# Optimization experiments

Hardware: AMD Instinct MI355X
Metric: run time of the kernel (lower is better)

The kernel has to match this reference:

```python
import jax, jax.numpy as jnp
from jax import lax
import numpy as np

N_QUBITS = 8
N_LAYERS = 7
DIM = 2 ** N_QUBITS  # 256 amplitudes


def _conv(x, w, b, stride, pad):
    y = lax.conv_general_dilated(x, w, (stride, stride), [(pad, pad), (pad, pad)],
                                 dimension_numbers=("NCHW", "OIHW", "NCHW"))
    return y + b[None, :, None, None]


def _adaptive_pool2(x):
    # AdaptiveAvgPool2d(2) on 7x7 input: bins [0:4) and [3:7) per spatial dim (overlap at idx 3)
    bins = [(0, 4), (3, 7)]
    rows = [x[:, :, s:e, :].mean(axis=2) for s, e in bins]  # each (B,C,7)
    return jnp.stack([jnp.stack([r[:, :, s:e].mean(axis=2) for s, e in bins], axis=-1)
                      for r in rows], axis=-2)  # (B,C,2,2)


def _qsim(feat, weights):
    # Batched 8-qubit statevector simulation. PennyLane default.qubit ordering:
    # wire 0 is the most-significant axis. RY and CNOT are real matrices and the
    # amplitude-embedded state is real, so the state stays real throughout.
    norm = jnp.linalg.norm(feat, axis=1, keepdims=True)
    state = feat / jnp.maximum(norm, 1e-12)  # AmplitudeEmbedding(normalize=True), (B,256)
    B = state.shape[0]
    for layer in range(N_LAYERS):
        for q in range(N_QUBITS):  # RY(weights[layer,q]) on wire q
            theta = weights[layer, q]
            c, s = jnp.cos(theta / 2), jnp.sin(theta / 2)
            st = state.reshape(B, 2 ** q, 2, 2 ** (N_QUBITS - 1 - q))
            s0, s1 = st[:, :, 0, :], st[:, :, 1, :]
            state = jnp.stack([c * s0 - s * s1, s * s0 + c * s1], axis=2).reshape(B, DIM)
        for q in range(N_QUBITS - 1):  # CNOT(control=q, target=q+1)
            st = state.reshape(B, 2 ** q, 2, 2, 2 ** (N_QUBITS - 2 - q))
            swapped = st[:, :, 1, ::-1, :]  # flip target where control=1
            state = jnp.stack([st[:, :, 0], swapped], axis=2).reshape(B, DIM)
    st = state.reshape(B, 2, DIM // 2)
    return jnp.sum(st[:, 0] ** 2, axis=1) - jnp.sum(st[:, 1] ** 2, axis=1)  # <Z_0>


def setup_inputs() -> dict:
    key = jax.random.key(0)
    ks = jax.random.split(key, 24)
    B = 65536
    f32 = jnp.float32
    def nrm(k, shape, scale):
        return jax.random.normal(k, shape, f32) * scale
    return {
        "x": jax.random.normal(ks[0], (B, 1, 28, 28), f32),
        "conv1_w": nrm(ks[1], (3, 1, 5, 5), 0.2), "conv1_b": nrm(ks[2], (3,), 0.1),
        "conv2_w": nrm(ks[3], (6, 3, 3, 3), 0.2), "conv2_b": nrm(ks[4], (6,), 0.1),
        "conv3_w": nrm(ks[5], (12, 6, 3, 3), 0.2), "conv3_b": nrm(ks[6], (12,), 0.1),
        "fc_w": nrm(ks[7], (256, 48), 0.15), "fc_b": nrm(ks[8], (256,), 0.1),
        "q_weights": jax.random.uniform(ks[9], (N_LAYERS, N_QUBITS), f32, 0.0, 2.0 * np.pi),
        "cls1_w": nrm(ks[10], (180, 1), 0.5), "cls1_b": nrm(ks[11], (180,), 0.1),
        "cls2_w": nrm(ks[12], (140, 180), 0.08), "cls2_b": nrm(ks[13], (140,), 0.1),
        "cls3_w": nrm(ks[14], (100, 140), 0.09), "cls3_b": nrm(ks[15], (100,), 0.1),
        "cls4_w": nrm(ks[16], (50, 100), 0.1), "cls4_b": nrm(ks[17], (50,), 0.1),
        "cls5_w": nrm(ks[18], (1, 50), 0.15), "cls5_b": nrm(ks[19], (1,), 0.1),
    }


def reference(x, conv1_w, conv1_b, conv2_w, conv2_b, conv3_w, conv3_b, fc_w, fc_b,
              q_weights, cls1_w, cls1_b, cls2_w, cls2_b, cls3_w, cls3_b,
              cls4_w, cls4_b, cls5_w, cls5_b):
    h = jax.nn.relu(_conv(x, conv1_w, conv1_b, 2, 2))   # (B,3,14,14)
    h = jax.nn.relu(_conv(h, conv2_w, conv2_b, 2, 1))   # (B,6,7,7)
    h = jax.nn.relu(_conv(h, conv3_w, conv3_b, 1, 1))   # (B,12,7,7)
    h = _adaptive_pool2(h).reshape(h.shape[0], -1)      # (B,48)
    feat = jax.nn.relu(h @ fc_w.T + fc_b)               # (B,256); dropout = identity (eval)
    feat = feat / jnp.maximum(jnp.linalg.norm(feat, axis=1, keepdims=True), 1e-12)  # F.normalize
    qout = _qsim(feat, q_weights)[:, None]              # (B,1)
    h = jax.nn.relu(qout @ cls1_w.T + cls1_b)
    h = jax.nn.relu(h @ cls2_w.T + cls2_b)
    h = jax.nn.relu(h @ cls3_w.T + cls3_b)
    h = jax.nn.relu(h @ cls4_w.T + cls4_b)
    return jax.nn.sigmoid(h @ cls5_w.T + cls5_b)        # (B,1)
```

## Files before the change

### kernel.cpp

```cpp
#include <hip/hip_runtime.h>
#include <math.h>


#define WR2_SZ 1664
#define NL   16384
#define POOL_OFF (NL + 128)

constexpr int QM[7][8] = {
 {0x80,0x40,0x20,0x10,0x08,0x04,0x02,0x01},
 {0xC0,0x60,0x30,0x18,0x0C,0x06,0x03,0x01},
 {0xA0,0x50,0x28,0x14,0x0A,0x05,0x02,0x01},
 {0xF0,0x78,0x3C,0x1E,0x0F,0x07,0x03,0x01},
 {0x88,0x44,0x22,0x11,0x08,0x04,0x02,0x01},
 {0xCC,0x66,0x33,0x19,0x0C,0x06,0x03,0x01},
 {0xAA,0x55,0x2A,0x15,0x0A,0x05,0x02,0x01}};
constexpr int QR[7][8] = {
 {0x80,0x40,0x20,0x10,0x08,0x04,0x02,0x01},
 {0x80,0xC0,0xE0,0xF0,0xF8,0xFC,0xFE,0xFF},
 {0x80,0x40,0xA0,0x50,0xA8,0x54,0xAA,0x55},
 {0x80,0xC0,0x60,0x30,0x98,0xCC,0x66,0x33},
 {0x80,0x40,0x20,0x10,0x88,0x44,0x22,0x11},
 {0x80,0xC0,0xE0,0xF0,0x78,0x3C,0x1E,0x0F},
 {0x80,0x40,0xA0,0x50,0x28,0x14,0x0A,0x05}};

#define ROTSTEP2(L, Q) { \
    constexpr int m_  = QM[L][Q]; \
    constexpr int r_  = QR[L][Q]; \
    constexpr int lm_ = m_ >> 2, rm_ = m_ & 3; \
    constexpr int rl_ = r_ >> 2, rr_ = r_ & 3; \
    constexpr float f1_ = (rr_ & 1) ? -1.f : 1.f; \
    constexpr float f2_ = (rr_ & 2) ? -1.f : 1.f; \
    constexpr float f3_ = f1_ * f2_; \
    const float c_ = qtc[(L) * 8 + (Q)]; \
    const float s_ = qts[(L) * 8 + (Q)]; \
    float sgn_; \
    if constexpr (rl_ != 0) sgn_ = (__popc(lane & rl_) & 1) ? s_ : -s_; \
    else                    sgn_ = -s_; \
    float2 pU0_ = sU[0 ^ rm_], pU1_ = sU[1 ^ rm_], pU2_ = sU[2 ^ rm_], pU3_ = sU[3 ^ rm_]; \
    float2 pV0_ = sV[0 ^ rm_], pV1_ = sV[1 ^ rm_], pV2_ = sV[2 ^ rm_], pV3_ = sV[3 ^ rm_]; \
    if constexpr (lm_ != 0) { \
        pU0_.x = __shfl_xor(pU0_.x, lm_); pU0_.y = __shfl_xor(pU0_.y, lm_); \
        pU1_.x = __shfl_xor(pU1_.x, lm_); pU1_.y = __shfl_xor(pU1_.y, lm_); \
        pU2_.x = __shfl_xor(pU2_.x, lm_); pU2_.y = __shfl_xor(pU2_.y, lm_); \
        pU3_.x = __shfl_xor(pU3_.x, lm_); pU3_.y = __shfl_xor(pU3_.y, lm_); \
        pV0_.x = __shfl_xor(pV0_.x, lm_); pV0_.y = __shfl_xor(pV0_.y, lm_); \
        pV1_.x = __shfl_xor(pV1_.x, lm_); pV1_.y = __shfl_xor(pV1_.y, lm_); \
        pV2_.x = __shfl_xor(pV2_.x, lm_); pV2_.y = __shfl_xor(pV2_.y, lm_); \
        pV3_.x = __shfl_xor(pV3_.x, lm_); pV3_.y = __shfl_xor(pV3_.y, lm_); \
    } \
    sU[0].x = fmaf(c_, sU[0].x, sgn_ * pU0_.x); \
    sU[0].y = fmaf(c_, sU[0].y, sgn_ * pU0_.y); \
    sU[1].x = fmaf(c_, sU[1].x, (f1_ * sgn_) * pU1_.x); \
    sU[1].y = fmaf(c_, sU[1].y, (f1_ * sgn_) * pU1_.y); \
    sU[2].x = fmaf(c_, sU[2].x, (f2_ * sgn_) * pU2_.x); \
    sU[2].y = fmaf(c_, sU[2].y, (f2_ * sgn_) * pU2_.y); \
    sU[3].x = fmaf(c_, sU[3].x, (f3_ * sgn_) * pU3_.x); \
    sU[3].y = fmaf(c_, sU[3].y, (f3_ * sgn_) * pU3_.y); \
    sV[0].x = fmaf(c_, sV[0].x, sgn_ * pV0_.x); \
    sV[0].y = fmaf(c_, sV[0].y, sgn_ * pV0_.y); \
    sV[1].x = fmaf(c_, sV[1].x, (f1_ * sgn_) * pV1_.x); \
    sV[1].y = fmaf(c_, sV[1].y, (f1_ * sgn_) * pV1_.y); \
    sV[2].x = fmaf(c_, sV[2].x, (f2_ * sgn_) * pV2_.x); \
    sV[2].y = fmaf(c_, sV[2].y, (f2_ * sgn_) * pV2_.y); \
    sV[3].x = fmaf(c_, sV[3].x, (f3_ * sgn_) * pV3_.x); \
    sV[3].y = fmaf(c_, sV[3].y, (f3_ * sgn_) * pV3_.y); \
}

#define ROTLAYER2(L) \
    ROTSTEP2(L,0) ROTSTEP2(L,1) ROTSTEP2(L,2) ROTSTEP2(L,3) \
    ROTSTEP2(L,4) ROTSTEP2(L,5) ROTSTEP2(L,6) ROTSTEP2(L,7)

__global__ __launch_bounds__(256)
void build_lut(const float* __restrict__ w1, const float* __restrict__ b1,
               const float* __restrict__ w2, const float* __restrict__ b2,
               const float* __restrict__ w3, const float* __restrict__ b3,
               const float* __restrict__ w4, const float* __restrict__ b4,
               const float* __restrict__ w5, const float* __restrict__ b5,
               const float* __restrict__ qw,
               float* __restrict__ lut)
{
    __shared__ float hh[16][344];
    const int tid = threadIdx.x;
    const int e = tid >> 4;
    const int w = tid & 15;
    const int idx = blockIdx.x * 16 + e;
    const float t = -1.f + 2.f * (float)idx / (float)(NL - 1);

    if (blockIdx.x == 0 && tid < 56) {
        float th = 0.5f * qw[tid];
        lut[NL + tid]      = cosf(th);
        lut[NL + 56 + tid] = sinf(th);
    }

    float* hA = hh[e];
    float* hB = hA + 184;

    #pragma unroll
    for (int tt = 0; tt < 12; ++tt) {
        int j = tt * 16 + w;
        if (j < 180) hA[j] = fmaxf(fmaf(t, w1[j], b1[j]), 0.f);
    }
    for (int tt = 0; tt < 9; ++tt) {
        int j = tt * 16 + w;
        int jj = (j < 140) ? j : 0;
        const float4* wrow = (const float4*)(w2 + jj * 180);
        float a0 = 0.f, a1 = 0.f, a2 = 0.f, a3 = 0.f;
        for (int kc = 0; kc < 45; ++kc) {
            float4 h4 = *(const float4*)(hA + kc * 4);
            float4 ww = wrow[kc];
            a0 = fmaf(h4.x, ww.x, a0); a1 = fmaf(h4.y, ww.y, a1);
            a2 = fmaf(h4.z, ww.z, a2); a3 = fmaf(h4.w, ww.w, a3);
        }
        if (j < 140) hB[j] = fmaxf((a0 + a1) + (a2 + a3) + b2[j], 0.f);
    }
    for (int tt = 0; tt < 7; ++tt) {
        int j = tt * 16 + w;
        int jj = (j < 100) ? j : 0;
        const float4* wrow = (const float4*)(w3 + jj * 140);
        float a0 = 0.f, a1 = 0.f, a2 = 0.f, a3 = 0.f;
        for (int kc = 0; kc < 35; ++kc) {
            float4 h4 = *(const float4*)(hB + kc * 4);
            float4 ww = wrow[kc];
            a0 = fmaf(h4.x, ww.x, a0); a1 = fmaf(h4.y, ww.y, a1);
            a2 = fmaf(h4.z, ww.z, a2); a3 = fmaf(h4.w, ww.w, a3);
        }
        if (j < 100) hA[j] = fmaxf((a0 + a1) + (a2 + a3) + b3[j], 0.f);
    }
    for (int tt = 0; tt < 4; ++tt) {
        int j = tt * 16 + w;
        int jj = (j < 50) ? j : 0;
        const float4* wrow = (const float4*)(w4 + jj * 100);
        float a0 = 0.f, a1 = 0.f, a2 = 0.f, a3 = 0.f;
        for (int kc = 0; kc < 25; ++kc) {
            float4 h4 = *(const float4*)(hA + kc * 4);
            float4 ww = wrow[kc];
            a0 = fmaf(h4.x, ww.x, a0); a1 = fmaf(h4.y, ww.y, a1);
            a2 = fmaf(h4.z, ww.z, a2); a3 = fmaf(h4.w, ww.w, a3);
        }
        if (j < 50) hB[j] = fmaxf((a0 + a1) + (a2 + a3) + b4[j], 0.f);
    }
    float p5 = 0.f;
    for (int k = w; k < 50; k += 16) p5 = fmaf(hB[k], w5[k], p5);
    #pragma unroll
    for (int m = 1; m < 16; m <<= 1) p5 += __shfl_xor(p5, m);
    if (w == 0) lut[idx] = p5 + b5[0];
}

__global__ __launch_bounds__(256, 3)
void conv_pool(const float* __restrict__ x,
               const float* __restrict__ c1w, const float* __restrict__ c1b,
               const float* __restrict__ c2w, const float* __restrict__ c2b,
               const float* __restrict__ c3w, const float* __restrict__ c3b,
               float* __restrict__ poolg, int B)
{
    __shared__ float2 wreg2[4][WR2_SZ];

    const int tid  = threadIdx.x;
    const int lane = tid & 63;
    const int wv   = tid >> 6;

    float2* wr2 = wreg2[wv];
    const int base = blockIdx.x * 16;

    float2* c1p2  = wr2;
    float2* pin2  = wr2 + 672;
    float2* c2pT2 = wr2 + 672;
    float2* c3_2  = wr2;

    for (int pr = 0; pr < 2; ++pr) {
        const int sa = base + wv * 4 + pr * 2;
        if (sa >= B) break;
        const int sb = (sa + 1 < B) ? sa + 1 : sa;

        {
            float4 z4 = {0.f, 0.f, 0.f, 0.f};
            float* w0 = (float*)wr2;
            #pragma unroll
            for (int t = 0; t < 13; ++t)
                *(float4*)(w0 + t * 256 + lane * 4) = z4;
        }
        {
            const float4* xsA = (const float4*)(x + (size_t)sa * 784);
            const float4* xsB = (const float4*)(x + (size_t)sb * 784);
            #pragma unroll
            for (int t = 0; t < 4; ++t) {
                int i4 = t * 64 + lane;
                if (i4 < 196) {
                    float4 va = xsA[i4];
                    float4 vb = xsB[i4];
                    int r = i4 / 7;
                    int c = (i4 % 7) * 4;
                    float2* dst = pin2 + (r + 2) * 32 + (c + 2);
                    dst[0] = make_float2(va.x, vb.x);
                    dst[1] = make_float2(va.y, vb.y);
                    dst[2] = make_float2(va.z, vb.z);
                    dst[3] = make_float2(va.w, vb.w);
                }
            }
        }

        #pragma unroll
        for (int t = 0; t < 4; ++t) {
            int p = t * 64 + lane;
            bool valid = p < 196;
            int pp = valid ? p : 0;
            int y = pp / 14, xx = pp % 14;
            const float2* pr2 = pin2 + (2 * y) * 32 + 2 * xx;
            float2 win[25];
            #pragma unroll
            for (int ky = 0; ky < 5; ++ky) {
                const float2* rw = pr2 + ky * 32;
                #pragma unroll
                for (int j = 0; j < 5; ++j) win[ky * 5 + j] = rw[j];
            }
            #pragma unroll
            for (int c = 0; c < 3; ++c) {
                float ax = c1b[c], ay = c1b[c];
                #pragma unroll
                for (int k = 0; k < 25; ++k) {
                    float wk = c1w[c * 25 + k];
                    ax = fmaf(win[k].x, wk, ax);
                    ay = fmaf(win[k].y, wk, ay);
                }
                if (valid)
                    c1p2[c * 224 + y * 16 + (xx + 1)] =
                        make_float2(fmaxf(ax, 0.f), fmaxf(ay, 0.f));
            }
        }

        {
            float4 z4 = {0.f, 0.f, 0.f, 0.f};
            float4* zz = (float4*)c2pT2;
            #pragma unroll
            for (int t = 0; t < 6; ++t) {
                int i = t * 64 + lane;
                if (i < 324) zz[i] = z4;
            }
        }
        {
            int p = lane;
            bool valid = p < 49;
            int pp = valid ? p : 0;
            int y = pp / 7, xx = pp % 7;
            float acx[6], acy[6];
            #pragma unroll
            for (int c = 0; c < 6; ++c) { acx[c] = c2b[c]; acy[c] = c2b[c]; }
            #pragma unroll
            for (int ic = 0; ic < 3; ++ic) {
                const float2* bic = c1p2 + ic * 224;
                float2 win[9];
                #pragma unroll
                for (int ky = 0; ky < 3; ++ky) {
                    int rr = 2 * y - 1 + ky;
                    bool okr = rr >= 0;
                    int rc = okr ? rr : 0;
                    const float2* rw = bic + rc * 16 + 2 * xx;
                    float2 a0 = rw[0], a1 = rw[1], a2 = rw[2];
                    float2 z2 = {0.f, 0.f};
                    win[ky * 3 + 0] = okr ? a0 : z2;
                    win[ky * 3 + 1] = okr ? a1 : z2;
                    win[ky * 3 + 2] = okr ? a2 : z2;
                }
                #pragma unroll
                for (int c = 0; c < 6; ++c)
                    #pragma unroll
                    for (int k = 0; k < 9; ++k) {
                        float wk = c2w[c * 27 + ic * 9 + k];
                        acx[c] = fmaf(win[k].x, wk, acx[c]);
                        acy[c] = fmaf(win[k].y, wk, acy[c]);
                    }
            }
            if (valid) {
                float2* op = c2pT2 + ((y + 1) * 9 + (xx + 1)) * 8;
                #pragma unroll
                for (int c = 0; c < 6; ++c)
                    op[c] = make_float2(fmaxf(acx[c], 0.f), fmaxf(acy[c], 0.f));
            }
        }

        {
            int p = lane;
            bool valid = p < 49;
            int pp = valid ? p : 0;
            int y = pp / 7, xx = pp % 7;
            float acx[12], acy[12];
            #pragma unroll
            for (int c = 0; c < 12; ++c) { acx[c] = c3b[c]; acy[c] = c3b[c]; }
            #pragma unroll
            for (int dy = 0; dy < 3; ++dy)
                #pragma unroll
                for (int dx = 0; dx < 3; ++dx) {
                    const float2* cp = c2pT2 + ((y + dy) * 9 + (xx + dx)) * 8;
                    float2 ch[6];
                    #pragma unroll
                    for (int j = 0; j < 6; ++j) ch[j] = cp[j];
                    const int k = dy * 3 + dx;
                    #pragma unroll
                    for (int c = 0; c < 12; ++c) {
                        const float* wp = c3w + c * 54 + k;
                        #pragma unroll
                        for (int j = 0; j < 6; ++j) {
                            float wk = wp[j * 9];
                            acx[c] = fmaf(ch[j].x, wk, acx[c]);
                            acy[c] = fmaf(ch[j].y, wk, acy[c]);
                        }
                    }
                }
            if (valid) {
                #pragma unroll
                for (int c = 0; c < 12; ++c)
                    c3_2[c * 49 + p] = make_float2(fmaxf(acx[c], 0.f), fmaxf(acy[c], 0.f));
            }
        }

        {
            int o = lane;
            if (o < 48) {
                int c = o >> 2, i = (o >> 1) & 1, j = o & 1;
                int ri = i * 3, cj = j * 3;
                float sx = 0.f, sy = 0.f;
                #pragma unroll
                for (int dy = 0; dy < 4; ++dy)
                    #pragma unroll
                    for (int dx = 0; dx < 4; ++dx) {
                        float2 v = c3_2[c * 49 + (ri + dy) * 7 + (cj + dx)];
                        sx += v.x; sy += v.y;
                    }
                poolg[(size_t)sa * 48 + o] = sx * (1.f / 16.f);
                if (sb != sa) poolg[(size_t)sb * 48 + o] = sy * (1.f / 16.f);
            }
        }
    }
}

__global__ __launch_bounds__(256)
void qsim_cls(const float* __restrict__ fcw, const float* __restrict__ fcb,
              const float* __restrict__ lut, const float* __restrict__ poolg,
              float* __restrict__ out, int B)
{
    const int tid  = threadIdx.x;
    const int lane = tid & 63;
    const int wv   = tid >> 6;

    const float* qtc = lut + NL;
    const float* qts = lut + NL + 56;

    const int s0 = blockIdx.x * 16 + wv * 4;
    const int sa = (s0 + 0 < B) ? s0 + 0 : B - 1;
    const int sb = (s0 + 1 < B) ? s0 + 1 : B - 1;
    const int sc_ = (s0 + 2 < B) ? s0 + 2 : B - 1;
    const int sd = (s0 + 3 < B) ? s0 + 3 : B - 1;

    const float4* pvA = (const float4*)(poolg + (size_t)sa * 48);
    const float4* pvB = (const float4*)(poolg + (size_t)sb * 48);
    const float4* pvC = (const float4*)(poolg + (size_t)sc_ * 48);
    const float4* pvD = (const float4*)(poolg + (size_t)sd * 48);

    const int o0 = lane * 4;
    const float4* wr0 = (const float4*)(fcw + (o0 + 0) * 48);
    const float4* wr1 = (const float4*)(fcw + (o0 + 1) * 48);
    const float4* wr2 = (const float4*)(fcw + (o0 + 2) * 48);
    const float4* wr3 = (const float4*)(fcw + (o0 + 3) * 48);

    float2 aU[4], aV[4];
    #pragma unroll
    for (int j = 0; j < 4; ++j) { aU[j] = make_float2(0.f, 0.f); aV[j] = make_float2(0.f, 0.f); }

    #pragma unroll
    for (int kc = 0; kc < 12; ++kc) {
        float4 w0 = wr0[kc], w1 = wr1[kc], w2 = wr2[kc], w3 = wr3[kc];
        float4 vA = pvA[kc], vB = pvB[kc], vC = pvC[kc], vD = pvD[kc];
        aU[0].x = fmaf(vA.x, w0.x, fmaf(vA.y, w0.y, fmaf(vA.z, w0.z, fmaf(vA.w, w0.w, aU[0].x))));
        aU[0].y = fmaf(vB.x, w0.x, fmaf(vB.y, w0.y, fmaf(vB.z, w0.z, fmaf(vB.w, w0.w, aU[0].y))));
        aU[1].x = fmaf(vA.x, w1.x, fmaf(vA.y, w1.y, fmaf(vA.z, w1.z, fmaf(vA.w, w1.w, aU[1].x))));
        aU[1].y = fmaf(vB.x, w1.x, fmaf(vB.y, w1.y, fmaf(vB.z, w1.z, fmaf(vB.w, w1.w, aU[1].y))));
        aU[2].x = fmaf(vA.x, w2.x, fmaf(vA.y, w2.y, fmaf(vA.z, w2.z, fmaf(vA.w, w2.w, aU[2].x))));
        aU[2].y = fmaf(vB.x, w2.x, fmaf(vB.y, w2.y, fmaf(vB.z, w2.z, fmaf(vB.w, w2.w, aU[2].y))));
        aU[3].x = fmaf(vA.x, w3.x, fmaf(vA.y, w3.y, fmaf(vA.z, w3.z, fmaf(vA.w, w3.w, aU[3].x))));
        aU[3].y = fmaf(vB.x, w3.x, fmaf(vB.y, w3.y, fmaf(vB.z, w3.z, fmaf(vB.w, w3.w, aU[3].y))));
        aV[0].x = fmaf(vC.x, w0.x, fmaf(vC.y, w0.y, fmaf(vC.z, w0.z, fmaf(vC.w, w0.w, aV[0].x))));
        aV[0].y = fmaf(vD.x, w0.x, fmaf(vD.y, w0.y, fmaf(vD.z, w0.z, fmaf(vD.w, w0.w, aV[0].y))));
        aV[1].x = fmaf(vC.x, w1.x, fmaf(vC.y, w1.y, fmaf(vC.z, w1.z, fmaf(vC.w, w1.w, aV[1].x))));
        aV[1].y = fmaf(vD.x, w1.x, fmaf(vD.y, w1.y, fmaf(vD.z, w1.z, fmaf(vD.w, w1.w, aV[1].y))));
        aV[2].x = fmaf(vC.x, w2.x, fmaf(vC.y, w2.y, fmaf(vC.z, w2.z, fmaf(vC.w, w2.w, aV[2].x))));
        aV[2].y = fmaf(vD.x, w2.x, fmaf(vD.y, w2.y, fmaf(vD.z, w2.z, fmaf(vD.w, w2.w, aV[2].y))));
        aV[3].x = fmaf(vC.x, w3.x, fmaf(vC.y, w3.y, fmaf(vC.z, w3.z, fmaf(vC.w, w3.w, aV[3].x))));
        aV[3].y = fmaf(vD.x, w3.x, fmaf(vD.y, w3.y, fmaf(vD.z, w3.z, fmaf(vD.w, w3.w, aV[3].y))));
    }

    float4 fb = *(const float4*)(fcb + o0);
    const float fbv[4] = {fb.x, fb.y, fb.z, fb.w};

    float2 sU[4], sV[4];
    {
        float2 ssU = make_float2(0.f, 0.f), ssV = make_float2(0.f, 0.f);
        #pragma unroll
        for (int j = 0; j < 4; ++j) {
            sU[j].x = fmaxf(aU[j].x + fbv[j], 0.f);
            sU[j].y = fmaxf(aU[j].y + fbv[j], 0.f);
            sV[j].x = fmaxf(aV[j].x + fbv[j], 0.f);
            sV[j].y = fmaxf(aV[j].y + fbv[j], 0.f);
            ssU.x = fmaf(sU[j].x, sU[j].x, ssU.x);
            ssU.y = fmaf(sU[j].y, sU[j].y, ssU.y);
            ssV.x = fmaf(sV[j].x, sV[j].x, ssV.x);
            ssV.y = fmaf(sV[j].y, sV[j].y, ssV.y);
        }
        #pragma unroll
        for (int m = 1; m < 64; m <<= 1) {
            ssU.x += __shfl_xor(ssU.x, m); ssU.y += __shfl_xor(ssU.y, m);
            ssV.x += __shfl_xor(ssV.x, m); ssV.y += __shfl_xor(ssV.y, m);
        }
        float scUx = 1.f / fmaxf(sqrtf(ssU.x), 1e-12f);
        float scUy = 1.f / fmaxf(sqrtf(ssU.y), 1e-12f);
        float scVx = 1.f / fmaxf(sqrtf(ssV.x), 1e-12f);
        float scVy = 1.f / fmaxf(sqrtf(ssV.y), 1e-12f);
        #pragma unroll
        for (int j = 0; j < 4; ++j) {
            sU[j].x *= scUx; sU[j].y *= scUy;
            sV[j].x *= scVx; sV[j].y *= scVy;
        }
    }

    ROTLAYER2(0) ROTLAYER2(1) ROTLAYER2(2) ROTLAYER2(3)
    ROTLAYER2(4) ROTLAYER2(5) ROTLAYER2(6)

    float2 pU, pV;
    pU.x = sU[0].x*sU[0].x + sU[1].x*sU[1].x + sU[2].x*sU[2].x + sU[3].x*sU[3].x;
    pU.y = sU[0].y*sU[0].y + sU[1].y*sU[1].y + sU[2].y*sU[2].y + sU[3].y*sU[3].y;
    pV.x = sV[0].x*sV[0].x + sV[1].x*sV[1].x + sV[2].x*sV[2].x + sV[3].x*sV[3].x;
    pV.y = sV[0].y*sV[0].y + sV[1].y*sV[1].y + sV[2].y*sV[2].y + sV[3].y*sV[3].y;
    if (lane & 32) { pU.x = -pU.x; pU.y = -pU.y; pV.x = -pV.x; pV.y = -pV.y; }
    #pragma unroll
    for (int m = 1; m < 64; m <<= 1) {
        pU.x += __shfl_xor(pU.x, m); pU.y += __shfl_xor(pU.y, m);
        pV.x += __shfl_xor(pV.x, m); pV.y += __shfl_xor(pV.y, m);
    }

    if (lane < 4) {
        float qout = (lane == 0) ? pU.x : (lane == 1) ? pU.y : (lane == 2) ? pV.x : pV.y;
        int osample = s0 + lane;
        float u = (qout + 1.f) * 0.5f * (float)(NL - 1);
        int i0 = (int)floorf(u);
        i0 = (i0 < 0) ? 0 : ((i0 > NL - 2) ? NL - 2 : i0);
        float fr = u - (float)i0;
        float z0 = lut[i0], z1 = lut[i0 + 1];
        float z = fmaf(z1 - z0, fr, z0);
        if (osample < B) out[osample] = 1.f / (1.f + expf(-z));
    }
}

extern "C" void kernel_launch(void* const* d_in, const int* in_sizes, int n_in,
                              void* d_out, int out_size, void* d_ws, size_t ws_size,
                              hipStream_t stream) {
    const float* x   = (const float*)d_in[0];
    const float* c1w = (const float*)d_in[1];
    const float* c1b = (const float*)d_in[2];
    const float* c2w = (const float*)d_in[3];
    const float* c2b = (const float*)d_in[4];
    const float* c3w = (const float*)d_in[5];
    const float* c3b = (const float*)d_in[6];
    const float* fcw = (const float*)d_in[7];
    const float* fcb = (const float*)d_in[8];
    const float* qw  = (const float*)d_in[9];
    const float* w1  = (const float*)d_in[10];
    const float* b1  = (const float*)d_in[11];
    const float* w2  = (const float*)d_in[12];
    const float* b2  = (const float*)d_in[13];
    const float* w3  = (const float*)d_in[14];
    const float* b3  = (const float*)d_in[15];
    const float* w4  = (const float*)d_in[16];
    const float* b4  = (const float*)d_in[17];
    const float* w5  = (const float*)d_in[18];
    const float* b5  = (const float*)d_in[19];

    float* lut   = (float*)d_ws;
    float* poolg = (float*)d_ws + POOL_OFF;

    int B = in_sizes[0] / 784;

    build_lut<<<dim3(NL / 16), dim3(256), 0, stream>>>(
        w1, b1, w2, b2, w3, b3, w4, b4, w5, b5, qw, lut);

    int grid = (B + 15) / 16;
    conv_pool<<<dim3(grid), dim3(256), 0, stream>>>(
        x, c1w, c1b, c2w, c2b, c3w, c3b, poolg, B);

    qsim_cls<<<dim3(grid), dim3(256), 0, stream>>>(
        fcw, fcb, lut, poolg, (float*)d_out, B);
}
```

Before: 500.6 us.

## Fuse conv/pool kernel with FC, quantum sim and classifier into one kernel

Merges the conv_pool and qsim_cls kernels into one kernel. Pooled features stay in shared memory and feed the FC layer, normalization and the rotation layers directly. This removes the global write and re-read of the 48-float pooled buffer and one kernel launch. The cost is that the fused kernel keeps FC weight pointers and the state registers live through the conv phase under launch_bounds(256,3). That adds register pressure and may cause spills.

```diff
diff --git a/kernel.cpp b/kernel.cpp
--- a/kernel.cpp
+++ b/kernel.cpp
@@ -4,7 +4,6 @@
 
 #define WR2_SZ 1664
 #define NL   16384
-#define POOL_OFF (NL + 128)
 
 constexpr int QM[7][8] = {
  {0x80,0x40,0x20,0x10,0x08,0x04,0x02,0x01},
@@ -147,11 +146,13 @@
 }
 
 __global__ __launch_bounds__(256, 3)
-void conv_pool(const float* __restrict__ x,
+void fused_all(const float* __restrict__ x,
                const float* __restrict__ c1w, const float* __restrict__ c1b,
                const float* __restrict__ c2w, const float* __restrict__ c2b,
                const float* __restrict__ c3w, const float* __restrict__ c3b,
-               float* __restrict__ poolg, int B)
+               const float* __restrict__ fcw, const float* __restrict__ fcb,
+               const float* __restrict__ lut,
+               float* __restrict__ out, int B)
 {
     __shared__ float2 wreg2[4][WR2_SZ];
 
@@ -159,17 +160,31 @@
     const int lane = tid & 63;
     const int wv   = tid >> 6;
 
+    const float* qtc = lut + NL;
+    const float* qts = lut + NL + 56;
+
     float2* wr2 = wreg2[wv];
     const int base = blockIdx.x * 16;
 
-    float2* c1p2  = wr2;
-    float2* pin2  = wr2 + 672;
-    float2* c2pT2 = wr2 + 672;
-    float2* c3_2  = wr2;
-
+    float2* c1p2    = wr2;
+    float2* pin2    = wr2 + 672;
+    float2* c2pT2   = wr2 + 672;
+    float2* c3_2    = wr2;
+    float2* pooled2 = wr2 + 600;
+
+    float2 sU[4], sV[4];
+
+    const int o0 = lane * 4;
+    const float4* fr0 = (const float4*)(fcw + (o0 + 0) * 48);
+    const float4* fr1 = (const float4*)(fcw + (o0 + 1) * 48);
+    const float4* fr2 = (const float4*)(fcw + (o0 + 2) * 48);
+    const float4* fr3 = (const float4*)(fcw + (o0 + 3) * 48);
+    const float4 fb = *(const float4*)(fcb + o0);
+
+    #pragma unroll
     for (int pr = 0; pr < 2; ++pr) {
-        const int sa = base + wv * 4 + pr * 2;
-        if (sa >= B) break;
+        int sa = base + wv * 4 + pr * 2;
+        sa = (sa < B) ? sa : B - 1;
         const int sb = (sa + 1 < B) ? sa + 1 : sa;
 
         {
@@ -326,98 +341,44 @@
                         float2 v = c3_2[c * 49 + (ri + dy) * 7 + (cj + dx)];
                         sx += v.x; sy += v.y;
                     }
-                poolg[(size_t)sa * 48 + o] = sx * (1.f / 16.f);
-                if (sb != sa) poolg[(size_t)sb * 48 + o] = sy * (1.f / 16.f);
-            }
-        }
-    }
-}
-
-__global__ __launch_bounds__(256)
-void qsim_cls(const float* __restrict__ fcw, const float* __restrict__ fcb,
-              const float* __restrict__ lut, const float* __restrict__ poolg,
-              float* __restrict__ out, int B)
-{
-    const int tid  = threadIdx.x;
-    const int lane = tid & 63;
-    const int wv   = tid >> 6;
-
-    const float* qtc = lut + NL;
-    const float* qts = lut + NL + 56;
-
-    const int s0 = blockIdx.x * 16 + wv * 4;
-    const int sa = (s0 + 0 < B) ? s0 + 0 : B - 1;
-    const int sb = (s0 + 1 < B) ? s0 + 1 : B - 1;
-    const int sc_ = (s0 + 2 < B) ? s0 + 2 : B - 1;
-    const int sd = (s0 + 3 < B) ? s0 + 3 : B - 1;
-
-    const float4* pvA = (const float4*)(poolg + (size_t)sa * 48);
-    const float4* pvB = (const float4*)(poolg + (size_t)sb * 48);
-    const float4* pvC = (const float4*)(poolg + (size_t)sc_ * 48);
-    const float4* pvD = (const float4*)(poolg + (size_t)sd * 48);
-
-    const int o0 = lane * 4;
-    const float4* wr0 = (const float4*)(fcw + (o0 + 0) * 48);
-    const float4* wr1 = (const float4*)(fcw + (o0 + 1) * 48);
-    const float4* wr2 = (const float4*)(fcw + (o0 + 2) * 48);
-    const float4* wr3 = (const float4*)(fcw + (o0 + 3) * 48);
-
-    float2 aU[4], aV[4];
-    #pragma unroll
-    for (int j = 0; j < 4; ++j) { aU[j] = make_float2(0.f, 0.f); aV[j] = make_float2(0.f, 0.f); }
-
-    #pragma unroll
-    for (int kc = 0; kc < 12; ++kc) {
-        float4 w0 = wr0[kc], w1 = wr1[kc], w2 = wr2[kc], w3 = wr3[kc];
-        float4 vA = pvA[kc], vB = pvB[kc], vC = pvC[kc], vD = pvD[kc];
-        aU[0].x = fmaf(vA.x, w0.x, fmaf(vA.y, w0.y, fmaf(vA.z, w0.z, fmaf(vA.w, w0.w, aU[0].x))));
-        aU[0].y = fmaf(vB.x, w0.x, fmaf(vB.y, w0.y, fmaf(vB.z, w0.z, fmaf(vB.w, w0.w, aU[0].y))));
-        aU[1].x = fmaf(vA.x, w1.x, fmaf(vA.y, w1.y, fmaf(vA.z, w1.z, fmaf(vA.w, w1.w, aU[1].x))));
-        aU[1].y = fmaf(vB.x, w1.x, fmaf(vB.y, w1.y, fmaf(vB.z, w1.z, fmaf(vB.w, w1.w, aU[1].y))));
-        aU[2].x = fmaf(vA.x, w2.x, fmaf(vA.y, w2.y, fmaf(vA.z, w2.z, fmaf(vA.w, w2.w, aU[2].x))));
-        aU[2].y = fmaf(vB.x, w2.x, fmaf(vB.y, w2.y, fmaf(vB.z, w2.z, fmaf(vB.w, w2.w, aU[2].y))));
-        aU[3].x = fmaf(vA.x, w3.x, fmaf(vA.y, w3.y, fmaf(vA.z, w3.z, fmaf(vA.w, w3.w, aU[3].x))));
-        aU[3].y = fmaf(vB.x, w3.x, fmaf(vB.y, w3.y, fmaf(vB.z, w3.z, fmaf(vB.w, w3.w, aU[3].y))));
-        aV[0].x = fmaf(vC.x, w0.x, fmaf(vC.y, w0.y, fmaf(vC.z, w0.z, fmaf(vC.w, w0.w, aV[0].x))));
-        aV[0].y = fmaf(vD.x, w0.x, fmaf(vD.y, w0.y, fmaf(vD.z, w0.z, fmaf(vD.w, w0.w, aV[0].y))));
-        aV[1].x = fmaf(vC.x, w1.x, fmaf(vC.y, w1.y, fmaf(vC.z, w1.z, fmaf(vC.w, w1.w, aV[1].x))));
-        aV[1].y = fmaf(vD.x, w1.x, fmaf(vD.y, w1.y, fmaf(vD.z, w1.z, fmaf(vD.w, w1.w, aV[1].y))));
-        aV[2].x = fmaf(vC.x, w2.x, fmaf(vC.y, w2.y, fmaf(vC.z, w2.z, fmaf(vC.w, w2.w, aV[2].x))));
-        aV[2].y = fmaf(vD.x, w2.x, fmaf(vD.y, w2.y, fmaf(vD.z, w2.z, fmaf(vD.w, w2.w, aV[2].y))));
-        aV[3].x = fmaf(vC.x, w3.x, fmaf(vC.y, w3.y, fmaf(vC.z, w3.z, fmaf(vC.w, w3.w, aV[3].x))));
-        aV[3].y = fmaf(vD.x, w3.x, fmaf(vD.y, w3.y, fmaf(vD.z, w3.z, fmaf(vD.w, w3.w, aV[3].y))));
-    }
-
-    float4 fb = *(const float4*)(fcb + o0);
-    const float fbv[4] = {fb.x, fb.y, fb.z, fb.w};
-
-    float2 sU[4], sV[4];
-    {
-        float2 ssU = make_float2(0.f, 0.f), ssV = make_float2(0.f, 0.f);
-        #pragma unroll
-        for (int j = 0; j < 4; ++j) {
-            sU[j].x = fmaxf(aU[j].x + fbv[j], 0.f);
-            sU[j].y = fmaxf(aU[j].y + fbv[j], 0.f);
-            sV[j].x = fmaxf(aV[j].x + fbv[j], 0.f);
-            sV[j].y = fmaxf(aV[j].y + fbv[j], 0.f);
-            ssU.x = fmaf(sU[j].x, sU[j].x, ssU.x);
-            ssU.y = fmaf(sU[j].y, sU[j].y, ssU.y);
-            ssV.x = fmaf(sV[j].x, sV[j].x, ssV.x);
-            ssV.y = fmaf(sV[j].y, sV[j].y, ssV.y);
-        }
-        #pragma unroll
-        for (int m = 1; m < 64; m <<= 1) {
-            ssU.x += __shfl_xor(ssU.x, m); ssU.y += __shfl_xor(ssU.y, m);
-            ssV.x += __shfl_xor(ssV.x, m); ssV.y += __shfl_xor(ssV.y, m);
-        }
-        float scUx = 1.f / fmaxf(sqrtf(ssU.x), 1e-12f);
-        float scUy = 1.f / fmaxf(sqrtf(ssU.y), 1e-12f);
-        float scVx = 1.f / fmaxf(sqrtf(ssV.x), 1e-12f);
-        float scVy = 1.f / fmaxf(sqrtf(ssV.y), 1e-12f);
-        #pragma unroll
-        for (int j = 0; j < 4; ++j) {
-            sU[j].x *= scUx; sU[j].y *= scUy;
-            sV[j].x *= scVx; sV[j].y *= scVy;
+                pooled2[o] = make_float2(sx * (1.f / 16.f), sy * (1.f / 16.f));
+            }
+        }
+
+        {
+            float2 a0 = {0.f, 0.f}, a1 = {0.f, 0.f}, a2 = {0.f, 0.f}, a3 = {0.f, 0.f};
+            #pragma unroll
+            for (int kc = 0; kc < 12; ++kc) {
+                float4 w0 = fr0[kc], w1 = fr1[kc], w2 = fr2[kc], w3 = fr3[kc];
+                const float2* pv = pooled2 + kc * 4;
+                float2 p0 = pv[0], p1 = pv[1], p2 = pv[2], p3 = pv[3];
+                a0.x = fmaf(p0.x, w0.x, fmaf(p1.x, w0.y, fmaf(p2.x, w0.z, fmaf(p3.x, w0.w, a0.x))));
+                a0.y = fmaf(p0.y, w0.x, fmaf(p1.y, w0.y, fmaf(p2.y, w0.z, fmaf(p3.y, w0.w, a0.y))));
+                a1.x = fmaf(p0.x, w1.x, fmaf(p1.x, w1.y, fmaf(p2.x, w1.z, fmaf(p3.x, w1.w, a1.x))));
+                a1.y = fmaf(p0.y, w1.x, fmaf(p1.y, w1.y, fmaf(p2.y, w1.z, fmaf(p3.y, w1.w, a1.y))));
+                a2.x = fmaf(p0.x, w2.x, fmaf(p1.x, w2.y, fmaf(p2.x, w2.z, fmaf(p3.x, w2.w, a2.x))));
+                a2.y = fmaf(p0.y, w2.x, fmaf(p1.y, w2.y, fmaf(p2.y, w2.z, fmaf(p3.y, w2.w, a2.y))));
+                a3.x = fmaf(p0.x, w3.x, fmaf(p1.x, w3.y, fmaf(p2.x, w3.z, fmaf(p3.x, w3.w, a3.x))));
+                a3.y = fmaf(p0.y, w3.x, fmaf(p1.y, w3.y, fmaf(p2.y, w3.z, fmaf(p3.y, w3.w, a3.y))));
+            }
+            float2 t0, t1, t2, t3;
+            t0.x = fmaxf(a0.x + fb.x, 0.f); t0.y = fmaxf(a0.y + fb.x, 0.f);
+            t1.x = fmaxf(a1.x + fb.y, 0.f); t1.y = fmaxf(a1.y + fb.y, 0.f);
+            t2.x = fmaxf(a2.x + fb.z, 0.f); t2.y = fmaxf(a2.y + fb.z, 0.f);
+            t3.x = fmaxf(a3.x + fb.w, 0.f); t3.y = fmaxf(a3.y + fb.w, 0.f);
+            float ssx = fmaf(t0.x, t0.x, fmaf(t1.x, t1.x, fmaf(t2.x, t2.x, t3.x * t3.x)));
+            float ssy = fmaf(t0.y, t0.y, fmaf(t1.y, t1.y, fmaf(t2.y, t2.y, t3.y * t3.y)));
+            #pragma unroll
+            for (int m = 1; m < 64; m <<= 1) {
+                ssx += __shfl_xor(ssx, m);
+                ssy += __shfl_xor(ssy, m);
+            }
+            float scx = 1.f / fmaxf(sqrtf(ssx), 1e-12f);
+            float scy = 1.f / fmaxf(sqrtf(ssy), 1e-12f);
+            t0.x *= scx; t1.x *= scx; t2.x *= scx; t3.x *= scx;
+            t0.y *= scy; t1.y *= scy; t2.y *= scy; t3.y *= scy;
+            if (pr == 0) { sU[0] = t0; sU[1] = t1; sU[2] = t2; sU[3] = t3; }
+            else         { sV[0] = t0; sV[1] = t1; sV[2] = t2; sV[3] = t3; }
         }
     }
 
@@ -438,7 +399,7 @@
 
     if (lane < 4) {
         float qout = (lane == 0) ? pU.x : (lane == 1) ? pU.y : (lane == 2) ? pV.x : pV.y;
-        int osample = s0 + lane;
+        int osample = base + wv * 4 + lane;
         float u = (qout + 1.f) * 0.5f * (float)(NL - 1);
         int i0 = (int)floorf(u);
         i0 = (i0 < 0) ? 0 : ((i0 > NL - 2) ? NL - 2 : i0);
@@ -473,8 +434,7 @@
     const float* w5  = (const float*)d_in[18];
     const float* b5  = (const float*)d_in[19];
 
-    float* lut   = (float*)d_ws;
-    float* poolg = (float*)d_ws + POOL_OFF;
+    float* lut = (float*)d_ws;
 
     int B = in_sizes[0] / 784;
 
@@ -482,9 +442,7 @@
         w1, b1, w2, b2, w3, b3, w4, b4, w5, b5, qw, lut);
 
     int grid = (B + 15) / 16;
-    conv_pool<<<dim3(grid), dim3(256), 0, stream>>>(
-        x, c1w, c1b, c2w, c2b, c3w, c3b, poolg, B);
-
-    qsim_cls<<<dim3(grid), dim3(256), 0, stream>>>(
-        fcw, fcb, lut, poolg, (float*)d_out, B);
+    fused_all<<<dim3(grid), dim3(256), 0, stream>>>(
+        x, c1w, c1b, c2w, c2b, c3w, c3b, fcw, fcb, lut,
+        (float*)d_out, B);
 }
```

After: 478.4 us. 1.05x faster.
